# Performance work log

Hardware: AMD Instinct MI355X
Metric: run time of the kernel (lower is better)

The kernel has to match this reference:

```python
import jax, jax.numpy as jnp
import numpy as np

HUGE = jnp.float32(1e31)   # ops.HUGE_INT
EPS = 1e-20
B, AN = 1024, 256
D = 256            # emb_dim
HD = 512           # history_dim
AD = 2 * D         # action_dim
NE, NR = 100000, 400


def setup_inputs() -> dict:
    key = jax.random.key(0)
    ks = jax.random.split(key, 12)
    e = jax.random.randint(ks[0], (B,), 0, NE)
    q = jax.random.randint(ks[1], (B,), 0, NR)
    hstate = jax.random.normal(ks[2], (B, HD), dtype=jnp.float32)
    r_space = jax.random.randint(ks[3], (B, AN), 0, NR)
    e_space = jax.random.randint(ks[4], (B, AN), 0, NE)
    # binary action mask; guarantee at least one valid action per row
    action_mask = (jax.random.uniform(ks[5], (B, AN)) > 0.2).astype(jnp.float32)
    action_mask = action_mask.at[:, 0].set(1.0)
    entity_emb = jax.random.normal(ks[6], (NE, D), dtype=jnp.float32) * 0.02
    relation_emb = jax.random.normal(ks[7], (NR, D), dtype=jnp.float32) * 0.02
    W1 = jax.random.normal(ks[8], (2 * D + HD, AD), dtype=jnp.float32) * (1.0 / np.sqrt(2 * D + HD))
    b1 = jnp.zeros((AD,), dtype=jnp.float32)
    W2 = jax.random.normal(ks[9], (AD, AD), dtype=jnp.float32) * (1.0 / np.sqrt(AD))
    b2 = jnp.zeros((AD,), dtype=jnp.float32)
    return {"e": e, "q": q, "hstate": hstate, "r_space": r_space,
            "e_space": e_space, "action_mask": action_mask,
            "entity_emb": entity_emb, "relation_emb": relation_emb,
            "W1": W1, "b1": b1, "W2": W2, "b2": b2}


def reference(e, q, hstate, r_space, e_space, action_mask,
              entity_emb, relation_emb, W1, b1, W2, b2):
    Q = relation_emb[q]                       # [B, D]
    E = entity_emb[e]                         # [B, D]
    X = jnp.concatenate([E, hstate, Q], axis=-1)          # [B, 2D+HD]
    X = jax.nn.relu(X @ W1 + b1)                          # [B, AD]
    X2 = X @ W2 + b2                                      # [B, AD]
    # action embeddings: [rel_emb[r]; ent_emb[e]] per padded action slot
    A = jnp.concatenate([relation_emb[r_space], entity_emb[e_space]], axis=-1)  # [B, AN, AD]
    scores = jnp.einsum('bad,bd->ba', A, X2) - (1.0 - action_mask) * HUGE      # [B, AN]
    action_dist = jax.nn.softmax(scores, axis=-1)
    entropy = -jnp.sum(action_dist * jnp.log(jnp.clip(action_dist, EPS)), axis=-1)  # [B]
    return action_dist, entropy
```

## Files before the change

### kernel.cpp

```cpp
#include <hip/hip_runtime.h>
#include <math.h>

#define NB   1024
#define NACT 256
#define DIM  256
#define HDIM 512
#define ADIM 512
#define KTOT 1024
#define NE   100000
#define NR   400
#define NRP  448
#define G1B  128

typedef __attribute__((ext_vector_type(8))) short bf16x8;
typedef __attribute__((ext_vector_type(4))) float f32x4;

__device__ __forceinline__ unsigned short f2bf(float f) {
    unsigned int u = __float_as_uint(f);
    u += 0x7FFF + ((u >> 16) & 1);
    return (unsigned short)(u >> 16);
}
__device__ __forceinline__ float bf2f(unsigned short u) {
    return __uint_as_float(((unsigned int)u) << 16);
}
__device__ __forceinline__ ushort4 cvt4(float4 v) {
    ushort4 o = {f2bf(v.x), f2bf(v.y), f2bf(v.z), f2bf(v.w)};
    return o;
}

__global__ __launch_bounds__(256) void prep_transpose(
    const float* __restrict__ W1, const float* __restrict__ W2,
    ushort* __restrict__ W1T, ushort* __restrict__ W2T)
{
    __shared__ float t[64][68];
    const int z = blockIdx.z;
    if (z && blockIdx.x >= 8) return;
    const int Kd = z ? 512 : 1024;
    const float* in = z ? W2 : W1;
    ushort* out = z ? W2T : W1T;
    const int k0 = blockIdx.x * 64, n0 = blockIdx.y * 64;
    const int tid = threadIdx.x;
    const int kr = tid >> 2, c = tid & 3;
    #pragma unroll
    for (int j = 0; j < 4; ++j) {
        const float4 v = *(const float4*)(in + (size_t)(k0 + kr) * ADIM + n0 + c * 16 + j * 4);
        *(float4*)&t[kr][c * 16 + j * 4] = v;
    }
    __syncthreads();
    const int nr = tid >> 2;
    ushort tmp[16];
    #pragma unroll
    for (int kk = 0; kk < 16; ++kk) tmp[kk] = f2bf(t[c * 16 + kk][nr]);
    *(uint4*)(out + (size_t)(n0 + nr) * Kd + k0 + c * 16)     = *(uint4*)&tmp[0];
    *(uint4*)(out + (size_t)(n0 + nr) * Kd + k0 + c * 16 + 8) = *(uint4*)&tmp[8];
}

__global__ __launch_bounds__(256) void mega_conv_gemm1(
    const float* __restrict__ ent, const float* __restrict__ rel,
    const float* __restrict__ hstate,
    const int* __restrict__ e, const int* __restrict__ q,
    const ushort* __restrict__ W1T, const float* __restrict__ b1,
    ushort* __restrict__ entbf, ushort* __restrict__ relbf,
    ushort* __restrict__ Hbf)
{
    const int blk = blockIdx.x, tid = threadIdx.x;
    __shared__ __align__(16) ushort Als[64][40];
    __shared__ __align__(16) ushort Bls[64][40];

    if (blk >= G1B) {
        const int cb = blk - G1B;
        const float4* src = (const float4*)ent;
        ushort4* dst = (ushort4*)entbf;
        const int start = cb * 6250;
        const int end = start + 6250;
        int j = start + tid;
        for (; j + 768 < end; j += 1024) {
            const float4 v0 = src[j];
            const float4 v1 = src[j + 256];
            const float4 v2 = src[j + 512];
            const float4 v3 = src[j + 768];
            dst[j]       = cvt4(v0);
            dst[j + 256] = cvt4(v1);
            dst[j + 512] = cvt4(v2);
            dst[j + 768] = cvt4(v3);
        }
        for (; j < end; j += 256) dst[j] = cvt4(src[j]);
        if (cb < 100) {
            const int k = cb * 256 + tid;
            ((ushort4*)relbf)[k] = cvt4(((const float4*)rel)[k]);
        }
        return;
    }

    const int g  = blk;
    const int n0 = (g & 7) * 64;
    const int m0 = (g >> 3) * 64;
    const int wave = tid >> 6, lane = tid & 63;
    const int qq   = lane >> 4, l15 = lane & 15;
    const int sm   = tid >> 2, sc = tid & 3;
    const int kofs = sc * 8;

    const int row   = m0 + sm;
    const float* rowE = ent + (size_t)e[row] * DIM;
    const float* rowH = hstate + (size_t)row * HDIM - DIM;
    const float* rowQ = rel + (size_t)q[row] * DIM - (DIM + HDIM);
    const uint4* gb = (const uint4*)(W1T + (size_t)(n0 + sm) * KTOT) + sc;

    f32x4 acc[4];
    #pragma unroll
    for (int mt = 0; mt < 4; ++mt) acc[mt] = (f32x4){0.f, 0.f, 0.f, 0.f};

    float4 pa0 = *(const float4*)(rowE + kofs);
    float4 pa1 = *(const float4*)(rowE + kofs + 4);
    uint4  pb  = gb[0];

    for (int it = 0; it < KTOT / 32; ++it) {
        ushort t8[8];
        t8[0] = f2bf(pa0.x); t8[1] = f2bf(pa0.y); t8[2] = f2bf(pa0.z); t8[3] = f2bf(pa0.w);
        t8[4] = f2bf(pa1.x); t8[5] = f2bf(pa1.y); t8[6] = f2bf(pa1.z); t8[7] = f2bf(pa1.w);
        *(uint4*)&Als[sm][sc * 8] = *(uint4*)t8;
        *(uint4*)&Bls[sm][sc * 8] = pb;
        __syncthreads();
        if (it + 1 < KTOT / 32) {
            const int kg = (it + 1) * 32 + kofs;
            const float* src = (kg < DIM) ? rowE : ((kg < DIM + HDIM) ? rowH : rowQ);
            pa0 = *(const float4*)(src + kg);
            pa1 = *(const float4*)(src + kg + 4);
            pb  = gb[(it + 1) * 4];
        }
        const bf16x8 bfrag = *(const bf16x8*)&Bls[wave * 16 + l15][qq * 8];
        #pragma unroll
        for (int mt = 0; mt < 4; ++mt) {
            const bf16x8 afrag = *(const bf16x8*)&Als[mt * 16 + l15][qq * 8];
            acc[mt] = __builtin_amdgcn_mfma_f32_16x16x32_bf16(afrag, bfrag, acc[mt], 0, 0, 0);
        }
        __syncthreads();
    }
    const int n = n0 + wave * 16 + l15;
    const float bv = b1[n];
    #pragma unroll
    for (int mt = 0; mt < 4; ++mt)
        #pragma unroll
        for (int r = 0; r < 4; ++r) {
            const int m = m0 + mt * 16 + qq * 4 + r;
            Hbf[(size_t)m * ADIM + n] = f2bf(fmaxf(acc[mt][r] + bv, 0.0f));
        }
}

__global__ __launch_bounds__(256) void gemm2_mfma(
    const ushort* __restrict__ A, const ushort* __restrict__ Bt,
    const float* __restrict__ bias, float* __restrict__ Cf,
    ushort* __restrict__ X2rbf)
{
    __shared__ __align__(16) ushort Als[64][40];
    __shared__ __align__(16) ushort Bls[64][40];
    const int tid  = threadIdx.x;
    const int n0   = blockIdx.x * 64;
    const int m0   = blockIdx.y * 64;
    const int wave = tid >> 6, lane = tid & 63;
    const int qq   = lane >> 4, l15 = lane & 15;
    const int sm   = tid >> 2, sc = tid & 3;

    const uint4* ga = (const uint4*)(A  + (size_t)(m0 + sm) * ADIM) + sc;
    const uint4* gb = (const uint4*)(Bt + (size_t)(n0 + sm) * ADIM) + sc;

    f32x4 acc[4];
    #pragma unroll
    for (int mt = 0; mt < 4; ++mt) acc[mt] = (f32x4){0.f, 0.f, 0.f, 0.f};

    uint4 pa = ga[0], pb = gb[0];
    for (int it = 0; it < ADIM / 32; ++it) {
        *(uint4*)&Als[sm][sc * 8] = pa;
        *(uint4*)&Bls[sm][sc * 8] = pb;
        __syncthreads();
        if (it + 1 < ADIM / 32) {
            pa = ga[(it + 1) * 4];
            pb = gb[(it + 1) * 4];
        }
        const bf16x8 bfrag = *(const bf16x8*)&Bls[wave * 16 + l15][qq * 8];
        #pragma unroll
        for (int mt = 0; mt < 4; ++mt) {
            const bf16x8 afrag = *(const bf16x8*)&Als[mt * 16 + l15][qq * 8];
            acc[mt] = __builtin_amdgcn_mfma_f32_16x16x32_bf16(afrag, bfrag, acc[mt], 0, 0, 0);
        }
        __syncthreads();
    }
    const int n = n0 + wave * 16 + l15;
    const float bv = bias[n];
    const bool lowhalf = (n0 < 256);
    #pragma unroll
    for (int mt = 0; mt < 4; ++mt)
        #pragma unroll
        for (int r = 0; r < 4; ++r) {
            const int m = m0 + mt * 16 + qq * 4 + r;
            const float v = acc[mt][r] + bv;
            Cf[(size_t)m * ADIM + n] = v;
            if (lowhalf) X2rbf[(size_t)m * DIM + n] = f2bf(v);
        }
}

__global__ __launch_bounds__(256) void gemm_rel(
    const ushort* __restrict__ A, const ushort* __restrict__ Bt,
    float* __restrict__ R)
{
    __shared__ __align__(16) ushort Als[64][40];
    __shared__ __align__(16) ushort Bls[64][40];
    const int tid  = threadIdx.x;
    const int n0   = blockIdx.x * 64;
    const int m0   = blockIdx.y * 64;
    const int wave = tid >> 6, lane = tid & 63;
    const int qq   = lane >> 4, l15 = lane & 15;
    const int sm   = tid >> 2, sc = tid & 3;

    const int brow = (n0 + sm < NR) ? (n0 + sm) : (NR - 1);
    const uint4* ga = (const uint4*)(A  + (size_t)(m0 + sm) * DIM) + sc;
    const uint4* gb = (const uint4*)(Bt + (size_t)brow * DIM) + sc;

    f32x4 acc[4];
    #pragma unroll
    for (int mt = 0; mt < 4; ++mt) acc[mt] = (f32x4){0.f, 0.f, 0.f, 0.f};

    uint4 pa = ga[0], pb = gb[0];
    for (int it = 0; it < DIM / 32; ++it) {
        *(uint4*)&Als[sm][sc * 8] = pa;
        *(uint4*)&Bls[sm][sc * 8] = pb;
        __syncthreads();
        if (it + 1 < DIM / 32) {
            pa = ga[(it + 1) * 4];
            pb = gb[(it + 1) * 4];
        }
        const bf16x8 bfrag = *(const bf16x8*)&Bls[wave * 16 + l15][qq * 8];
        #pragma unroll
        for (int mt = 0; mt < 4; ++mt) {
            const bf16x8 afrag = *(const bf16x8*)&Als[mt * 16 + l15][qq * 8];
            acc[mt] = __builtin_amdgcn_mfma_f32_16x16x32_bf16(afrag, bfrag, acc[mt], 0, 0, 0);
        }
        __syncthreads();
    }
    const int n = n0 + wave * 16 + l15;
    if (n < NR) {
        #pragma unroll
        for (int mt = 0; mt < 4; ++mt)
            #pragma unroll
            for (int r = 0; r < 4; ++r) {
                const int m = m0 + mt * 16 + qq * 4 + r;
                R[(size_t)m * NRP + n] = acc[mt][r];
            }
    }
}

__global__ __launch_bounds__(512) void scores_kernel(
    const int* __restrict__ r_space, const int* __restrict__ e_space,
    const float* __restrict__ amask,
    const ushort* __restrict__ entbf, const float* __restrict__ R,
    const float* __restrict__ X2,
    float* __restrict__ dist_out, float* __restrict__ ent_out)
{
    const int b    = blockIdx.x;
    const int tid  = threadIdx.x;
    const int wave = tid >> 6;
    const int lane = tid & 63;

    __shared__ float xs[ADIM];
    __shared__ float sc[NACT];
    __shared__ int   ridx[NACT];
    __shared__ int   eidx[NACT];
    __shared__ float red1[8], red2[8], red3[8];

    if (tid < NACT) ridx[tid] = r_space[(size_t)b * NACT + tid];
    else            eidx[tid - NACT] = e_space[(size_t)b * NACT + tid - NACT];
    if (tid < ADIM / 4)
        ((float4*)xs)[tid] = ((const float4*)(X2 + (size_t)b * ADIM))[tid];
    __syncthreads();

    const float4 xe = ((const float4*)(xs + DIM))[lane];
    const float* R_row = R + (size_t)b * NRP;

    const int abase = wave * 32;
    for (int a0 = abase; a0 < abase + 32; a0 += 16) {
        const float rsc = (lane < 16) ? R_row[ridx[a0 + lane]] : 0.0f;
        ushort4 ev[16];
        #pragma unroll
        for (int i = 0; i < 16; ++i)
            ev[i] = ((const ushort4*)entbf)[(size_t)eidx[a0 + i] * (DIM / 4) + lane];
        float p[16];
        #pragma unroll
        for (int i = 0; i < 16; ++i) {
            p[i] = bf2f(ev[i].x) * xe.x + bf2f(ev[i].y) * xe.y
                 + bf2f(ev[i].z) * xe.z + bf2f(ev[i].w) * xe.w;
        }
        #pragma unroll
        for (int off = 32; off; off >>= 1) {
            #pragma unroll
            for (int i = 0; i < 16; ++i) p[i] += __shfl_xor(p[i], off);
        }
        float out = p[0];
        #pragma unroll
        for (int i = 1; i < 16; ++i) out = (lane == i) ? p[i] : out;
        if (lane < 16) sc[a0 + lane] = out + rsc;
    }
    __syncthreads();

    float s = -3.0e38f;
    if (tid < NACT) {
        const float m = amask[(size_t)b * NACT + tid];
        s = sc[tid] - (1.0f - m) * 1e31f;
    }

    float mx = s;
    #pragma unroll
    for (int off = 32; off; off >>= 1) mx = fmaxf(mx, __shfl_xor(mx, off));
    if (lane == 0) red1[wave] = mx;
    __syncthreads();
    mx = red1[0];
    #pragma unroll
    for (int w = 1; w < 8; ++w) mx = fmaxf(mx, red1[w]);

    const float ex = (tid < NACT) ? expf(s - mx) : 0.0f;
    float sum = ex;
    #pragma unroll
    for (int off = 32; off; off >>= 1) sum += __shfl_xor(sum, off);
    if (lane == 0) red2[wave] = sum;
    __syncthreads();
    sum = ((red2[0] + red2[1]) + (red2[2] + red2[3]))
        + ((red2[4] + red2[5]) + (red2[6] + red2[7]));

    const float d = ex / sum;
    if (tid < NACT) dist_out[(size_t)b * NACT + tid] = d;

    float t = (tid < NACT) ? d * logf(fmaxf(d, 1e-20f)) : 0.0f;
    #pragma unroll
    for (int off = 32; off; off >>= 1) t += __shfl_xor(t, off);
    if (lane == 0) red3[wave] = t;
    __syncthreads();
    if (tid == 0)
        ent_out[b] = -(((red3[0] + red3[1]) + (red3[2] + red3[3]))
                     + ((red3[4] + red3[5]) + (red3[6] + red3[7])));
}

extern "C" void kernel_launch(void* const* d_in, const int* in_sizes, int n_in,
                              void* d_out, int out_size, void* d_ws, size_t ws_size,
                              hipStream_t stream) {
    const int*   e       = (const int*)d_in[0];
    const int*   q       = (const int*)d_in[1];
    const float* hstate  = (const float*)d_in[2];
    const int*   r_space = (const int*)d_in[3];
    const int*   e_space = (const int*)d_in[4];
    const float* amask   = (const float*)d_in[5];
    const float* ent     = (const float*)d_in[6];
    const float* rel     = (const float*)d_in[7];
    const float* W1      = (const float*)d_in[8];
    const float* b1      = (const float*)d_in[9];
    const float* W2      = (const float*)d_in[10];
    const float* b2      = (const float*)d_in[11];

    ushort* W1T   = (ushort*)d_ws;
    ushort* W2T   = W1T   + (size_t)ADIM * KTOT;
    ushort* Hbf   = W2T   + (size_t)ADIM * ADIM;
    ushort* entbf = Hbf   + (size_t)NB * ADIM;
    ushort* relbf = entbf + (size_t)NE * DIM;
    float*  X2    = (float*)(relbf + (size_t)NR * DIM);
    ushort* X2rbf = (ushort*)(X2 + (size_t)NB * ADIM);
    float*  Rtab  = (float*)(X2rbf + (size_t)NB * DIM);
    float*  dist  = (float*)d_out;
    float*  entr  = dist + (size_t)NB * NACT;

    prep_transpose<<<dim3(16, 8, 2), 256, 0, stream>>>(W1, W2, W1T, W2T);
    mega_conv_gemm1<<<G1B + 1024, 256, 0, stream>>>(
        ent, rel, hstate, e, q, W1T, b1, entbf, relbf, Hbf);
    gemm2_mfma<<<dim3(ADIM / 64, NB / 64), 256, 0, stream>>>(Hbf, W2T, b2, X2, X2rbf);
    gemm_rel<<<dim3(NRP / 64, NB / 64), 256, 0, stream>>>(X2rbf, relbf, Rtab);
    scores_kernel<<<NB, 512, 0, stream>>>(
        r_space, e_space, amask, entbf, Rtab, X2, dist, entr);
}
```

Before: 234.8 us.

## Drop bf16 entity table conversion and gather fp32 entity rows directly

After: 228.1 us. 2.8% less time.

```diff
diff --git a/kernel.cpp b/kernel.cpp
--- a/kernel.cpp
+++ b/kernel.cpp
@@ -10,7 +10,6 @@
 #define NE   100000
 #define NR   400
 #define NRP  448
-#define G1B  128
 
 typedef __attribute__((ext_vector_type(8))) short bf16x8;
 typedef __attribute__((ext_vector_type(4))) float f32x4;
@@ -30,16 +29,25 @@
 
 __global__ __launch_bounds__(256) void prep_transpose(
     const float* __restrict__ W1, const float* __restrict__ W2,
-    ushort* __restrict__ W1T, ushort* __restrict__ W2T)
-{
+    const float* __restrict__ rel,
+    ushort* __restrict__ W1T, ushort* __restrict__ W2T,
+    ushort* __restrict__ relbf)
+{
+    const int z = blockIdx.z;
+    const int tid = threadIdx.x;
+    if (z == 2) {
+        const int flat = blockIdx.x * 8 + blockIdx.y;
+        const int j = flat * 200 + tid;
+        if (tid < 200)
+            ((ushort4*)relbf)[j] = cvt4(((const float4*)rel)[j]);
+        return;
+    }
     __shared__ float t[64][68];
-    const int z = blockIdx.z;
     if (z && blockIdx.x >= 8) return;
     const int Kd = z ? 512 : 1024;
     const float* in = z ? W2 : W1;
     ushort* out = z ? W2T : W1T;
     const int k0 = blockIdx.x * 64, n0 = blockIdx.y * 64;
-    const int tid = threadIdx.x;
     const int kr = tid >> 2, c = tid & 3;
     #pragma unroll
     for (int j = 0; j < 4; ++j) {
@@ -55,44 +63,18 @@
     *(uint4*)(out + (size_t)(n0 + nr) * Kd + k0 + c * 16 + 8) = *(uint4*)&tmp[8];
 }
 
-__global__ __launch_bounds__(256) void mega_conv_gemm1(
+__global__ __launch_bounds__(256) void gemm1_mfma(
     const float* __restrict__ ent, const float* __restrict__ rel,
     const float* __restrict__ hstate,
     const int* __restrict__ e, const int* __restrict__ q,
     const ushort* __restrict__ W1T, const float* __restrict__ b1,
-    ushort* __restrict__ entbf, ushort* __restrict__ relbf,
     ushort* __restrict__ Hbf)
 {
-    const int blk = blockIdx.x, tid = threadIdx.x;
+    const int tid = threadIdx.x;
     __shared__ __align__(16) ushort Als[64][40];
     __shared__ __align__(16) ushort Bls[64][40];
 
-    if (blk >= G1B) {
-        const int cb = blk - G1B;
-        const float4* src = (const float4*)ent;
-        ushort4* dst = (ushort4*)entbf;
-        const int start = cb * 6250;
-        const int end = start + 6250;
-        int j = start + tid;
-        for (; j + 768 < end; j += 1024) {
-            const float4 v0 = src[j];
-            const float4 v1 = src[j + 256];
-            const float4 v2 = src[j + 512];
-            const float4 v3 = src[j + 768];
-            dst[j]       = cvt4(v0);
-            dst[j + 256] = cvt4(v1);
-            dst[j + 512] = cvt4(v2);
-            dst[j + 768] = cvt4(v3);
-        }
-        for (; j < end; j += 256) dst[j] = cvt4(src[j]);
-        if (cb < 100) {
-            const int k = cb * 256 + tid;
-            ((ushort4*)relbf)[k] = cvt4(((const float4*)rel)[k]);
-        }
-        return;
-    }
-
-    const int g  = blk;
+    const int g  = blockIdx.x;
     const int n0 = (g & 7) * 64;
     const int m0 = (g >> 3) * 64;
     const int wave = tid >> 6, lane = tid & 63;
@@ -149,7 +131,7 @@
 
 __global__ __launch_bounds__(256) void gemm2_mfma(
     const ushort* __restrict__ A, const ushort* __restrict__ Bt,
-    const float* __restrict__ bias, float* __restrict__ Cf,
+    const float* __restrict__ bias, float* __restrict__ X2up,
     ushort* __restrict__ X2rbf)
 {
     __shared__ __align__(16) ushort Als[64][40];
@@ -187,15 +169,14 @@
     }
     const int n = n0 + wave * 16 + l15;
     const float bv = bias[n];
-    const bool lowhalf = (n0 < 256);
     #pragma unroll
     for (int mt = 0; mt < 4; ++mt)
         #pragma unroll
         for (int r = 0; r < 4; ++r) {
             const int m = m0 + mt * 16 + qq * 4 + r;
             const float v = acc[mt][r] + bv;
-            Cf[(size_t)m * ADIM + n] = v;
-            if (lowhalf) X2rbf[(size_t)m * DIM + n] = f2bf(v);
+            if (n < 256) X2rbf[(size_t)m * DIM + n] = f2bf(v);
+            else         X2up [(size_t)m * DIM + (n - 256)] = v;
         }
 }
 
@@ -252,8 +233,8 @@
 __global__ __launch_bounds__(512) void scores_kernel(
     const int* __restrict__ r_space, const int* __restrict__ e_space,
     const float* __restrict__ amask,
-    const ushort* __restrict__ entbf, const float* __restrict__ R,
-    const float* __restrict__ X2,
+    const float* __restrict__ ent, const float* __restrict__ R,
+    const float* __restrict__ X2up,
     float* __restrict__ dist_out, float* __restrict__ ent_out)
 {
     const int b    = blockIdx.x;
@@ -261,7 +242,7 @@
     const int wave = tid >> 6;
     const int lane = tid & 63;
 
-    __shared__ float xs[ADIM];
+    __shared__ float xs[DIM];
     __shared__ float sc[NACT];
     __shared__ int   ridx[NACT];
     __shared__ int   eidx[NACT];
@@ -269,26 +250,24 @@
 
     if (tid < NACT) ridx[tid] = r_space[(size_t)b * NACT + tid];
     else            eidx[tid - NACT] = e_space[(size_t)b * NACT + tid - NACT];
-    if (tid < ADIM / 4)
-        ((float4*)xs)[tid] = ((const float4*)(X2 + (size_t)b * ADIM))[tid];
-    __syncthreads();
-
-    const float4 xe = ((const float4*)(xs + DIM))[lane];
+    if (tid < DIM / 4)
+        ((float4*)xs)[tid] = ((const float4*)(X2up + (size_t)b * DIM))[tid];
+    __syncthreads();
+
+    const float4 xe = ((const float4*)xs)[lane];
     const float* R_row = R + (size_t)b * NRP;
 
     const int abase = wave * 32;
     for (int a0 = abase; a0 < abase + 32; a0 += 16) {
         const float rsc = (lane < 16) ? R_row[ridx[a0 + lane]] : 0.0f;
-        ushort4 ev[16];
+        float4 ev[16];
         #pragma unroll
         for (int i = 0; i < 16; ++i)
-            ev[i] = ((const ushort4*)entbf)[(size_t)eidx[a0 + i] * (DIM / 4) + lane];
+            ev[i] = ((const float4*)(ent + (size_t)eidx[a0 + i] * DIM))[lane];
         float p[16];
         #pragma unroll
-        for (int i = 0; i < 16; ++i) {
-            p[i] = bf2f(ev[i].x) * xe.x + bf2f(ev[i].y) * xe.y
-                 + bf2f(ev[i].z) * xe.z + bf2f(ev[i].w) * xe.w;
-        }
+        for (int i = 0; i < 16; ++i)
+            p[i] = ev[i].x * xe.x + ev[i].y * xe.y + ev[i].z * xe.z + ev[i].w * xe.w;
         #pragma unroll
         for (int off = 32; off; off >>= 1) {
             #pragma unroll
@@ -357,19 +336,17 @@
     ushort* W1T   = (ushort*)d_ws;
     ushort* W2T   = W1T   + (size_t)ADIM * KTOT;
     ushort* Hbf   = W2T   + (size_t)ADIM * ADIM;
-    ushort* entbf = Hbf   + (size_t)NB * ADIM;
-    ushort* relbf = entbf + (size_t)NE * DIM;
-    float*  X2    = (float*)(relbf + (size_t)NR * DIM);
-    ushort* X2rbf = (ushort*)(X2 + (size_t)NB * ADIM);
-    float*  Rtab  = (float*)(X2rbf + (size_t)NB * DIM);
+    ushort* relbf = Hbf   + (size_t)NB * ADIM;
+    ushort* X2rbf = relbf + (size_t)NR * DIM;
+    float*  X2up  = (float*)(X2rbf + (size_t)NB * DIM);
+    float*  Rtab  = X2up + (size_t)NB * DIM;
     float*  dist  = (float*)d_out;
     float*  entr  = dist + (size_t)NB * NACT;
 
-    prep_transpose<<<dim3(16, 8, 2), 256, 0, stream>>>(W1, W2, W1T, W2T);
-    mega_conv_gemm1<<<G1B + 1024, 256, 0, stream>>>(
-        ent, rel, hstate, e, q, W1T, b1, entbf, relbf, Hbf);
-    gemm2_mfma<<<dim3(ADIM / 64, NB / 64), 256, 0, stream>>>(Hbf, W2T, b2, X2, X2rbf);
+    prep_transpose<<<dim3(16, 8, 3), 256, 0, stream>>>(W1, W2, rel, W1T, W2T, relbf);
+    gemm1_mfma<<<128, 256, 0, stream>>>(ent, rel, hstate, e, q, W1T, b1, Hbf);
+    gemm2_mfma<<<dim3(ADIM / 64, NB / 64), 256, 0, stream>>>(Hbf, W2T, b2, X2up, X2rbf);
     gemm_rel<<<dim3(NRP / 64, NB / 64), 256, 0, stream>>>(X2rbf, relbf, Rtab);
     scores_kernel<<<NB, 512, 0, stream>>>(
-        r_space, e_space, amask, entbf, Rtab, X2, dist, entr);
-}
+        r_space, e_space, amask, ent, Rtab, X2up, dist, entr);
+}
```
